# Optimization experiments

Measured on AMD Instinct MI355X. Metric: run time of the kernel, lower is better.

## Reference

```python
import jax, jax.numpy as jnp
import numpy as np

SCALE = 64 ** (-0.5)  # dim_head**-0.5; heads/dim_head otherwise unused in forward


def setup_inputs() -> dict:
    key = jax.random.key(0)
    ks = jax.random.split(key, 7)
    B, C, T = 8, 512, 4096
    s = C ** (-0.5)  # conv1d default init scale-ish
    x = jax.random.normal(ks[0], (B, C, T), dtype=jnp.float32)
    Wq = jax.random.normal(ks[1], (C, C), dtype=jnp.float32) * s
    bq = jax.random.normal(ks[2], (C,), dtype=jnp.float32) * s
    Wk = jax.random.normal(ks[3], (C, C), dtype=jnp.float32) * s
    bk = jax.random.normal(ks[4], (C,), dtype=jnp.float32) * s
    Wv = jax.random.normal(ks[5], (C, C), dtype=jnp.float32) * s
    bv = jax.random.normal(ks[6], (C,), dtype=jnp.float32) * s
    return {"x": x, "Wq": Wq, "bq": bq, "Wk": Wk, "bk": bk, "Wv": Wv, "bv": bv}


def reference(x, Wq, bq, Wk, bk, Wv, bv):
    # 1x1 Conv1d == per-timestep linear over channels: (o,c) x (b,c,t) -> (b,o,t)
    q = jnp.einsum('oc,bct->bot', Wq, x) + bq[None, :, None]
    k = jnp.einsum('oc,bct->bot', Wk, x) + bk[None, :, None]
    v = jnp.einsum('oc,bct->bot', Wv, x) + bv[None, :, None]
    # Channel-channel attention: dots (b, C, C); softmax over last (channel) axis
    dots = jnp.einsum('bct,bdt->bcd', q, k) * SCALE
    attn = jax.nn.softmax(dots, axis=-1)
    # (b,C,C) x (b,C,t) -> (b,C,t); dropout p=0 and to_out unused in original forward
    out = jnp.einsum('bcd,bdt->bct', attn, v)
    return out
```

## Files before the change

kernel.cpp:

```cpp
#include <hip/hip_runtime.h>

#define B_ 8
#define C_ 512
#define T_ 4096

typedef __attribute__((ext_vector_type(8))) __bf16 bf16x8;
typedef __attribute__((ext_vector_type(8))) _Float16 f16x8;
typedef __attribute__((ext_vector_type(8))) unsigned short u16x8;
typedef __attribute__((ext_vector_type(4))) float f32x4;

__device__ __forceinline__ unsigned short f2bf(float f) {
  unsigned int u = __float_as_uint(f);
  u += 0x7fffu + ((u >> 16) & 1u);
  return (unsigned short)(u >> 16);
}
__device__ __forceinline__ float bf2f(unsigned short h) {
  return __uint_as_float(((unsigned int)h) << 16);
}
__device__ __forceinline__ unsigned short f2h(float f) {
  return __builtin_bit_cast(unsigned short, (_Float16)f);
}

__device__ __forceinline__ void async16(unsigned short* ldsdst, const unsigned short* gsrc) {
  __builtin_amdgcn_global_load_lds(
      (__attribute__((address_space(1))) void*)(void*)const_cast<unsigned short*>(gsrc),
      (__attribute__((address_space(3))) void*)(void*)ldsdst,
      16, 0, 0);
}

template <bool F16>
__device__ __forceinline__ f32x4 mfma16(u16x8 a, u16x8 b, f32x4 c) {
  if constexpr (F16)
    return __builtin_amdgcn_mfma_f32_16x16x32_f16(
        __builtin_bit_cast(f16x8, a), __builtin_bit_cast(f16x8, b), c, 0, 0, 0);
  else
    return __builtin_amdgcn_mfma_f32_16x16x32_bf16(
        __builtin_bit_cast(bf16x8, a), __builtin_bit_cast(bf16x8, b), c, 0, 0, 0);
}

struct GemmP {
  const unsigned short* Ah; const unsigned short* Al; long sA; int lda;
  const unsigned short* Bh; const unsigned short* Bl; long sB; int ldb;
  float* Cf; unsigned short* Ch; unsigned short* Cl; long sC; int ldc;
  int kspan; int zparts;
  const float* rowv; const float* colv; const float* bq; const float* bk;
};

enum { EPI_F32 = 0, EPI_OUT = 1, EPI_DOTS = 2, EPI_SPLIT = 3, EPI_F16 = 4 };

template <int BM, int BN, int WM, int WN, bool SA, bool SB, int EPI, bool F16, int SWZ>
__global__ __launch_bounds__((BM / WM) * (BN / WN) * 64) void gemm_nt(GemmP g) {
  constexpr int KC = 64;
  constexpr int NWAVE = (BM / WM) * (BN / WN);
  constexpr int NT = NWAVE * 64;
  constexpr int ASZ = BM * KC, BSZ = BN * KC;
  constexpr int STAGE = (SA ? 2 : 1) * ASZ + (SB ? 2 : 1) * BSZ;
  constexpr int EPAD = BN + 4;
  constexpr int EPIB = 32 * EPAD * 4;
  constexpr int LDSB = (STAGE * 2 > EPIB) ? STAGE * 2 : EPIB;
  __shared__ alignas(16) char ldsraw[LDSB];
  unsigned short* lds = (unsigned short*)ldsraw;
  unsigned short* ldsAh = lds;
  unsigned short* ldsAl = lds + ASZ;
  unsigned short* ldsBh = lds + (SA ? 2 : 1) * ASZ;
  unsigned short* ldsBl = ldsBh + BSZ;

  const int tid = threadIdx.x;
  const int lane = tid & 63, wid = tid >> 6;
  constexpr int WNB = BN / WN;
  const int wm = wid / WNB, wn = wid % WNB;
  constexpr int MF = WM / 16, NF = WN / 16;

  int bm, bn, z;
  if constexpr (SWZ == 1) {
    const int blk = blockIdx.x;
    const int r = blk & 7, q = blk >> 3;
    const int idx = ((r >> 2) * 40) + q;
    const int tri = idx % 10;
    const int tm = (tri >= 6) ? 3 : (tri >= 3) ? 2 : (tri >= 1) ? 1 : 0;
    bm = tm; bn = tri - (tm * (tm + 1)) / 2;
    z = (idx / 10) * 4 + (r & 3);
  } else if constexpr (SWZ == 2) {
    const int blk = blockIdx.x;
    const int r = blk & 7, q = blk >> 3;
    bm = q & 3;
    const int w = q >> 2;
    bn = ((w & 1) << 3) + r;
    z = w >> 1;
  } else {
    bm = blockIdx.x; bn = blockIdx.y; z = blockIdx.z;
  }
  const int b = z / g.zparts, kp = z - b * g.zparts;

  const unsigned short* Ah = g.Ah + (size_t)b * g.sA + (size_t)kp * g.kspan;
  const unsigned short* Al = SA ? (g.Al + (size_t)b * g.sA + (size_t)kp * g.kspan) : nullptr;
  const unsigned short* Bh = g.Bh + (size_t)b * g.sB + (size_t)kp * g.kspan;
  const unsigned short* Bl = SB ? (g.Bl + (size_t)b * g.sB + (size_t)kp * g.kspan) : nullptr;

  f32x4 acc[MF][NF] = {};

  const int kIters = g.kspan / KC;
  for (int kt = 0; kt < kIters; ++kt) {
    const int kb = kt * KC;
#pragma unroll
    for (int r = 0; r < ASZ / (8 * NT); ++r) {
      int idx = tid + r * NT;
      int row = idx >> 3, sl = idx & 7;
      int kc = (sl ^ (row & 7)) << 3;
      size_t goff = (size_t)(bm * BM + row) * g.lda + kb + kc;
      async16(&ldsAh[idx << 3], Ah + goff);
      if constexpr (SA) async16(&ldsAl[idx << 3], Al + goff);
    }
#pragma unroll
    for (int r = 0; r < BSZ / (8 * NT); ++r) {
      int idx = tid + r * NT;
      int row = idx >> 3, sl = idx & 7;
      int kc = (sl ^ (row & 7)) << 3;
      size_t goff = (size_t)(bn * BN + row) * g.ldb + kb + kc;
      async16(&ldsBh[idx << 3], Bh + goff);
      if constexpr (SB) async16(&ldsBl[idx << 3], Bl + goff);
    }
    __syncthreads();

    const int rsel = lane & 15, kq = lane >> 4;
#pragma unroll
    for (int ks = 0; ks < KC; ks += 32) {
      const int chunk = (ks >> 3) + kq;
      u16x8 afh[MF], afl[MF], bfh[NF], bfl[NF];
#pragma unroll
      for (int fm = 0; fm < MF; ++fm) {
        int row = wm * WM + fm * 16 + rsel;
        int ro = row * KC + ((chunk ^ (row & 7)) << 3);
        afh[fm] = *(const u16x8*)&ldsAh[ro];
        if constexpr (SA) afl[fm] = *(const u16x8*)&ldsAl[ro];
      }
#pragma unroll
      for (int fn = 0; fn < NF; ++fn) {
        int row = wn * WN + fn * 16 + rsel;
        int ro = row * KC + ((chunk ^ (row & 7)) << 3);
        bfh[fn] = *(const u16x8*)&ldsBh[ro];
        if constexpr (SB) bfl[fn] = *(const u16x8*)&ldsBl[ro];
      }
#pragma unroll
      for (int fm = 0; fm < MF; ++fm)
#pragma unroll
        for (int fn = 0; fn < NF; ++fn) {
          acc[fm][fn] = mfma16<F16>(afh[fm], bfh[fn], acc[fm][fn]);
          if constexpr (SB) acc[fm][fn] = mfma16<F16>(afh[fm], bfl[fn], acc[fm][fn]);
          if constexpr (SA) acc[fm][fn] = mfma16<F16>(afl[fm], bfh[fn], acc[fm][fn]);
        }
    }
    __syncthreads();
  }

  if constexpr (EPI == EPI_SPLIT || EPI == EPI_F16) {
#pragma unroll
    for (int fm = 0; fm < MF; ++fm)
#pragma unroll
      for (int fn = 0; fn < NF; ++fn)
#pragma unroll
        for (int r = 0; r < 4; ++r) {
          int i = bm * BM + wm * WM + fm * 16 + ((lane >> 4) << 2) + r;
          int j = bn * BN + wn * WN + fn * 16 + (lane & 15);
          float v = acc[fm][fn][r];
          size_t co = (size_t)z * g.sC + (size_t)i * g.ldc + j;
          if constexpr (EPI == EPI_SPLIT) {
            unsigned short h = f2bf(v);
            g.Ch[co] = h;
            g.Cl[co] = f2bf(v - bf2f(h));
          } else {
            g.Ch[co] = f2h(v);
          }
        }
  } else {
    float* eb = (float*)ldsraw;
#pragma unroll
    for (int ck = 0; ck < BM / 32; ++ck) {
      if (wm == (ck * 32) / WM) {
        const int fm0 = ((ck * 32) % WM) / 16;
#pragma unroll
        for (int fi = 0; fi < 2; ++fi) {
          int fm = fm0 + fi;
#pragma unroll
          for (int fn = 0; fn < NF; ++fn)
#pragma unroll
            for (int r = 0; r < 4; ++r) {
              int lrow = fi * 16 + ((lane >> 4) << 2) + r;
              int col = wn * WN + fn * 16 + (lane & 15);
              eb[lrow * EPAD + col] = acc[fm][fn][r];
            }
        }
      }
      __syncthreads();
#pragma unroll
      for (int it = 0; it < (32 * BN / 4) / NT; ++it) {
        int idx = it * NT + tid;
        int row = idx / (BN / 4), c4 = (idx % (BN / 4)) * 4;
        f32x4 v = *(f32x4*)&eb[row * EPAD + c4];
        int grow = bm * BM + ck * 32 + row;
        int j = bn * BN + c4;
        if constexpr (EPI == EPI_OUT) v = v + g.rowv[b * C_ + grow];
        if constexpr (EPI == EPI_DOTS) {
          f32x4 bkv = *(const f32x4*)&g.bk[j];
          f32x4 ksv = *(const f32x4*)&g.colv[b * C_ + j];
          float qsi = g.rowv[b * C_ + grow], bqi = g.bq[grow];
          v = 0.125f * (v + qsi * bkv + bqi * (ksv + 4096.f * bkv));
        }
        __builtin_nontemporal_store(
            v, (f32x4*)&g.Cf[(size_t)z * g.sC + (size_t)grow * g.ldc + j]);
      }
      __syncthreads();
    }
  }
}

#define NXB2 1024
#define PAD 66
__global__ __launch_bounds__(256) void prep_fused(
    const float* __restrict__ x, const float* __restrict__ Wq,
    const float* __restrict__ Wk, const float* __restrict__ Wv,
    unsigned short* __restrict__ Xh, unsigned short* __restrict__ XhT,
    unsigned short* Wqh, unsigned short* Wql,
    unsigned short* Wkh, unsigned short* Wkl, unsigned short* WvT,
    float* __restrict__ S) {
  __shared__ unsigned short tile[64 * PAD];
  const int tid = threadIdx.x;
  if (blockIdx.x < NXB2) {
    const int tl = blockIdx.x;
    const int tb = tl & 15, c0 = ((tl >> 4) & 7) << 6, b = tl >> 7;
    const int t0 = tb << 8;
    const float* xin = x + ((size_t)(b * C_ + c0)) * T_ + t0;
    unsigned short* xo = Xh + ((size_t)(b * C_ + c0)) * T_ + t0;
    const int row16 = tid >> 4, c4 = (tid & 15) << 2;
    float rs[4] = {};
    float4 v[4];
#pragma unroll
    for (int r = 0; r < 4; ++r)
      v[r] = *(const float4*)&xin[(size_t)(row16 + r * 16) * T_ + c4];
    for (int st = 0; st < 4; ++st) {
      if (st) __syncthreads();
#pragma unroll
      for (int r = 0; r < 4; ++r) {
        int row = row16 + r * 16;
        _Float16 q0 = (_Float16)v[r].x, q1 = (_Float16)v[r].y,
                 q2 = (_Float16)v[r].z, q3 = (_Float16)v[r].w;
        unsigned short h0 = __builtin_bit_cast(unsigned short, q0),
                       h1 = __builtin_bit_cast(unsigned short, q1),
                       h2 = __builtin_bit_cast(unsigned short, q2),
                       h3 = __builtin_bit_cast(unsigned short, q3);
        rs[r] += (float)q0 + (float)q1 + (float)q2 + (float)q3;
        ushort4 hv; hv.x = h0; hv.y = h1; hv.z = h2; hv.w = h3;
        *(ushort4*)&xo[(size_t)row * T_ + st * 64 + c4] = hv;
        unsigned int lo = (unsigned int)h0 | ((unsigned int)h1 << 16);
        unsigned int hi = (unsigned int)h2 | ((unsigned int)h3 << 16);
        ((unsigned int*)&tile[row * PAD + c4])[0] = lo;
        ((unsigned int*)&tile[row * PAD + c4])[1] = hi;
      }
      float4 nv[4];
      if (st < 3) {
#pragma unroll
        for (int r = 0; r < 4; ++r)
          nv[r] = *(const float4*)&xin[(size_t)(row16 + r * 16) * T_ + (st + 1) * 64 + c4];
      }
      __syncthreads();
#pragma unroll
      for (int r = 0; r < 2; ++r) {
        int idx = tid + r * 256;
        int trow = idx >> 3, cc = (idx & 7) << 3;
        unsigned short vals[8];
#pragma unroll
        for (int j = 0; j < 8; ++j) vals[j] = tile[(cc + j) * PAD + trow];
        *(uint4*)&XhT[((size_t)b * T_ + t0 + st * 64 + trow) * C_ + c0 + cc] =
            *(uint4*)vals;
      }
#pragma unroll
      for (int r = 0; r < 4; ++r) v[r] = nv[r];
    }
#pragma unroll
    for (int rr = 0; rr < 4; ++rr) {
      float s = rs[rr];
      s += __shfl_down(s, 8, 16);
      s += __shfl_down(s, 4, 16);
      s += __shfl_down(s, 2, 16);
      s += __shfl_down(s, 1, 16);
      if ((tid & 15) == 0) atomicAdd(&S[(b << 9) + c0 + row16 + rr * 16], s);
    }
  } else {
    int i = (blockIdx.x - NXB2) * 256 + tid;
    float q = Wq[i]; unsigned short qh = f2bf(q); Wqh[i] = qh; Wql[i] = f2bf(q - bf2f(qh));
    float k = Wk[i]; unsigned short kh = f2bf(k); Wkh[i] = kh; Wkl[i] = f2bf(k - bf2f(kh));
    float v = Wv[i]; int d = i >> 9, e = i & 511;
    WvT[(e << 9) + d] = f2h(v);
  }
}

__global__ __launch_bounds__(256) void combine_g(const float* __restrict__ gp,
                                                 unsigned short* __restrict__ gh,
                                                 unsigned short* __restrict__ gl) {
  __shared__ float tile[64 * 65];
  const int blk = blockIdx.x;
  const int b = blk & 7, q = blk >> 3;
  const int tr = q >> 3, tc = q & 7;
  const bool mirror = (tr >> 1) < (tc >> 1);
  const int sr = mirror ? tc : tr, sc = mirror ? tr : tc;
  const float* src = gp + ((size_t)b << 20) + (size_t)(sr << 6) * 512 + (sc << 6);
  const int row = threadIdx.x >> 4, c4 = (threadIdx.x & 15) << 2;
  float vals[4][4];
#pragma unroll
  for (int rr = 0; rr < 4; ++rr) {
    const int r = row + rr * 16;
    f32x4 v = {};
#pragma unroll
    for (int p = 0; p < 4; ++p)
      v += __builtin_nontemporal_load(
          (const f32x4*)&src[((size_t)p << 18) + (size_t)r * 512 + c4]);
    if (mirror) {
#pragma unroll
      for (int k = 0; k < 4; ++k) tile[r * 65 + c4 + k] = v[k];
    } else {
#pragma unroll
      for (int k = 0; k < 4; ++k) vals[rr][k] = v[k];
    }
  }
  if (mirror) {
    __syncthreads();
#pragma unroll
    for (int rr = 0; rr < 4; ++rr) {
      const int r = row + rr * 16;
#pragma unroll
      for (int k = 0; k < 4; ++k) vals[rr][k] = tile[(c4 + k) * 65 + r];
    }
  }
  unsigned short* ghp = gh + ((size_t)b << 18) + (size_t)(tr << 6) * 512 + (tc << 6);
  unsigned short* glp = gl + ((size_t)b << 18) + (size_t)(tr << 6) * 512 + (tc << 6);
#pragma unroll
  for (int rr = 0; rr < 4; ++rr) {
    const int r = row + rr * 16;
    ushort4 h, l;
    h.x = f2bf(vals[rr][0]); l.x = f2bf(vals[rr][0] - bf2f(h.x));
    h.y = f2bf(vals[rr][1]); l.y = f2bf(vals[rr][1] - bf2f(h.y));
    h.z = f2bf(vals[rr][2]); l.z = f2bf(vals[rr][2] - bf2f(h.z));
    h.w = f2bf(vals[rr][3]); l.w = f2bf(vals[rr][3] - bf2f(h.w));
    *(ushort4*)&ghp[(size_t)r * 512 + c4] = h;
    *(ushort4*)&glp[(size_t)r * 512 + c4] = l;
  }
}

__global__ __launch_bounds__(256) void qs_ks(const float* __restrict__ Wq, const float* __restrict__ Wk,
                                             const float* __restrict__ s, float* __restrict__ qs,
                                             float* __restrict__ ks) {
  int lane = threadIdx.x & 63, wid = threadIdx.x >> 6;
  int gi = blockIdx.x * 4 + wid;
  int b = gi >> 9, i = gi & 511;
  const float* sv = s + (b << 9);
  const float* wqr = Wq + (size_t)i * C_;
  const float* wkr = Wk + (size_t)i * C_;
  float aq = 0.f, ak = 0.f;
#pragma unroll
  for (int c = lane; c < C_; c += 64) {
    float sc = sv[c];
    aq += wqr[c] * sc;
    ak += wkr[c] * sc;
  }
#pragma unroll
  for (int o = 32; o > 0; o >>= 1) { aq += __shfl_down(aq, o); ak += __shfl_down(ak, o); }
  if (lane == 0) { qs[gi] = aq; ks[gi] = ak; }
}

__global__ __launch_bounds__(256) void softmax_rows(const float* __restrict__ logits,
                                                    const float* __restrict__ bv,
                                                    unsigned short* __restrict__ attn,
                                                    float* __restrict__ ab) {
  const int row = blockIdx.x;
  const int tid = threadIdx.x, lane = tid & 63, wid = tid >> 6;
  const float* L = logits + (size_t)row * C_;
  float v0 = __builtin_nontemporal_load(&L[tid]);
  float v1 = __builtin_nontemporal_load(&L[tid + 256]);
  __shared__ float red[4];
  float m = fmaxf(v0, v1);
#pragma unroll
  for (int o = 32; o > 0; o >>= 1) m = fmaxf(m, __shfl_down(m, o));
  if (lane == 0) red[wid] = m;
  __syncthreads();
  m = fmaxf(fmaxf(red[0], red[1]), fmaxf(red[2], red[3]));
  __syncthreads();
  float e0 = __expf(v0 - m), e1 = __expf(v1 - m);
  float sum = e0 + e1;
#pragma unroll
  for (int o = 32; o > 0; o >>= 1) sum += __shfl_down(sum, o);
  if (lane == 0) red[wid] = sum;
  __syncthreads();
  sum = red[0] + red[1] + red[2] + red[3];
  float inv = 1.f / sum;
  float a0 = e0 * inv, a1 = e1 * inv;
  unsigned short* ar = attn + (size_t)row * C_;
  ar[tid] = f2h(a0);
  ar[tid + 256] = f2h(a1);
  float abv = a0 * bv[tid] + a1 * bv[tid + 256];
  __syncthreads();
#pragma unroll
  for (int o = 32; o > 0; o >>= 1) abv += __shfl_down(abv, o);
  if (lane == 0) red[wid] = abv;
  __syncthreads();
  if (tid == 0) ab[row] = red[0] + red[1] + red[2] + red[3];
}

extern "C" void kernel_launch(void* const* d_in, const int* in_sizes, int n_in,
                              void* d_out, int out_size, void* d_ws, size_t ws_size,
                              hipStream_t stream) {
  const float* x  = (const float*)d_in[0];
  const float* Wq = (const float*)d_in[1];
  const float* bq = (const float*)d_in[2];
  const float* Wk = (const float*)d_in[3];
  const float* bk = (const float*)d_in[4];
  const float* Wv = (const float*)d_in[5];
  const float* bv = (const float*)d_in[6];
  float* out = (float*)d_out;

  char* ws = (char*)d_ws;
  size_t off = 0;
  auto alloc = [&](size_t bytes) {
    char* p = ws + off;
    off += (bytes + 255) & ~(size_t)255;
    return p;
  };
  const size_t XSZ = (size_t)B_ * C_ * T_;
  const size_t GSZ = (size_t)B_ * C_ * C_;

  unsigned short* Xh  = (unsigned short*)alloc(XSZ * 2);
  unsigned short* XhT = (unsigned short*)alloc(XSZ * 2);
  float* Gpart = (float*)alloc((size_t)4 * GSZ * 4);
  unsigned short* Gh = (unsigned short*)alloc(GSZ * 2);
  unsigned short* Gl = (unsigned short*)alloc(GSZ * 2);
  unsigned short* Ph = (unsigned short*)alloc(GSZ * 2);
  unsigned short* Pl = (unsigned short*)alloc(GSZ * 2);
  float* Logits = (float*)alloc(GSZ * 4);
  unsigned short* Attn = (unsigned short*)alloc(GSZ * 2);
  unsigned short* Mh = (unsigned short*)alloc(GSZ * 2);
  unsigned short* Wqh = (unsigned short*)alloc((size_t)C_ * C_ * 2);
  unsigned short* Wql = (unsigned short*)alloc((size_t)C_ * C_ * 2);
  unsigned short* Wkh = (unsigned short*)alloc((size_t)C_ * C_ * 2);
  unsigned short* Wkl = (unsigned short*)alloc((size_t)C_ * C_ * 2);
  unsigned short* WvT = (unsigned short*)alloc((size_t)C_ * C_ * 2);
  float* S  = (float*)alloc((size_t)B_ * C_ * 4);
  float* Qs = (float*)alloc((size_t)B_ * C_ * 4);
  float* Ks = (float*)alloc((size_t)B_ * C_ * 4);
  float* Ab = (float*)alloc((size_t)B_ * C_ * 4);

  hipMemsetAsync(S, 0, (size_t)B_ * C_ * 4, stream);
  prep_fused<<<NXB2 + C_ * C_ / 256, 256, 0, stream>>>(x, Wq, Wk, Wv, Xh, XhT,
                                                       Wqh, Wql, Wkh, Wkl, WvT, S);
  qs_ks<<<B_ * C_ / 4, 256, 0, stream>>>(Wq, Wk, S, Qs, Ks);

  {
    GemmP p = {};
    p.Ah = Xh; p.sA = (long)C_ * T_; p.lda = T_;
    p.Bh = Xh; p.sB = (long)C_ * T_; p.ldb = T_;
    p.Cf = Gpart; p.sC = (long)C_ * C_; p.ldc = C_;
    p.kspan = T_ / 4; p.zparts = 4;
    gemm_nt<128, 128, 32, 64, false, false, EPI_F32, true, 1>
        <<<320, 512, 0, stream>>>(p);
  }
  combine_g<<<B_ * 64, 256, 0, stream>>>(Gpart, Gh, Gl);

  {
    GemmP p = {};
    p.Ah = Wqh; p.Al = Wql; p.sA = 0; p.lda = C_;
    p.Bh = Gh; p.Bl = Gl; p.sB = (long)C_ * C_; p.ldb = C_;
    p.Ch = Ph; p.Cl = Pl; p.sC = (long)C_ * C_; p.ldc = C_;
    p.kspan = C_; p.zparts = 1;
    gemm_nt<64, 64, 32, 32, true, true, EPI_SPLIT, false, 0>
        <<<dim3(8, 8, 8), 256, 0, stream>>>(p);
  }
  {
    GemmP p = {};
    p.Ah = Ph; p.Al = Pl; p.sA = (long)C_ * C_; p.lda = C_;
    p.Bh = Wkh; p.Bl = Wkl; p.sB = 0; p.ldb = C_;
    p.Cf = Logits; p.sC = (long)C_ * C_; p.ldc = C_;
    p.kspan = C_; p.zparts = 1;
    p.rowv = Qs; p.colv = Ks; p.bq = bq; p.bk = bk;
    gemm_nt<64, 64, 32, 32, true, true, EPI_DOTS, false, 0>
        <<<dim3(8, 8, 8), 256, 0, stream>>>(p);
  }
  softmax_rows<<<B_ * C_, 256, 0, stream>>>(Logits, bv, Attn, Ab);
  {
    GemmP p = {};
    p.Ah = Attn; p.sA = (long)C_ * C_; p.lda = C_;
    p.Bh = WvT; p.sB = 0; p.ldb = C_;
    p.Ch = Mh; p.sC = (long)C_ * C_; p.ldc = C_;
    p.kspan = C_; p.zparts = 1;
    gemm_nt<64, 64, 32, 32, false, false, EPI_F16, true, 0>
        <<<dim3(8, 8, 8), 256, 0, stream>>>(p);
  }
  {
    GemmP p = {};
    p.Ah = Mh; p.sA = (long)C_ * C_; p.lda = C_;
    p.Bh = XhT; p.sB = (long)C_ * T_; p.ldb = C_;
    p.Cf = out; p.sC = (long)C_ * T_; p.ldc = T_;
    p.kspan = C_; p.zparts = 1;
    p.rowv = Ab;
    gemm_nt<128, 256, 64, 64, false, false, EPI_OUT, true, 2>
        <<<512, 512, 0, stream>>>(p);
  }
  (void)in_sizes; (void)n_in; (void)out_size; (void)ws_size;
}
```

Baseline: 233.7 us.

## Double-buffer LDS stages in gemm_nt and retile output GEMM to 128x128

Adds a two-stage LDS ping-pong so the next K-chunk's async global-to-LDS loads are issued before the current chunk's MFMA work, letting memory latency overlap compute. The LDS footprint doubles for every gemm_nt instantiation, which may lower occupancy. The final output GEMM also moves from 128x256 tiles on 512 blocks to 128x128 tiles on 1024 blocks, with a matching block-index swizzle. The barrier structure needs care: the loop body shown no longer has a barrier right after the prefetch, so correctness depends on the trailing __syncthreads and on waiting for the async copies.

```diff
diff --git a/kernel.cpp b/kernel.cpp
--- a/kernel.cpp
+++ b/kernel.cpp
@@ -57,13 +57,9 @@
   constexpr int STAGE = (SA ? 2 : 1) * ASZ + (SB ? 2 : 1) * BSZ;
   constexpr int EPAD = BN + 4;
   constexpr int EPIB = 32 * EPAD * 4;
-  constexpr int LDSB = (STAGE * 2 > EPIB) ? STAGE * 2 : EPIB;
+  constexpr int LDSB = (STAGE * 4 > EPIB) ? STAGE * 4 : EPIB;
   __shared__ alignas(16) char ldsraw[LDSB];
   unsigned short* lds = (unsigned short*)ldsraw;
-  unsigned short* ldsAh = lds;
-  unsigned short* ldsAl = lds + ASZ;
-  unsigned short* ldsBh = lds + (SA ? 2 : 1) * ASZ;
-  unsigned short* ldsBl = ldsBh + BSZ;
 
   const int tid = threadIdx.x;
   const int lane = tid & 63, wid = tid >> 6;
@@ -83,10 +79,9 @@
   } else if constexpr (SWZ == 2) {
     const int blk = blockIdx.x;
     const int r = blk & 7, q = blk >> 3;
-    bm = q & 3;
-    const int w = q >> 2;
-    bn = ((w & 1) << 3) + r;
-    z = w >> 1;
+    bn = ((q & 3) << 3) + r;
+    bm = (q >> 2) & 3;
+    z = q >> 4;
   } else {
     bm = blockIdx.x; bn = blockIdx.y; z = blockIdx.z;
   }
@@ -97,19 +92,19 @@
   const unsigned short* Bh = g.Bh + (size_t)b * g.sB + (size_t)kp * g.kspan;
   const unsigned short* Bl = SB ? (g.Bl + (size_t)b * g.sB + (size_t)kp * g.kspan) : nullptr;
 
-  f32x4 acc[MF][NF] = {};
-
-  const int kIters = g.kspan / KC;
-  for (int kt = 0; kt < kIters; ++kt) {
-    const int kb = kt * KC;
+  auto stage = [&](int half, int kb) {
+    unsigned short* dAh = lds + half * STAGE;
+    unsigned short* dAl = dAh + ASZ;
+    unsigned short* dBh = dAh + (SA ? 2 : 1) * ASZ;
+    unsigned short* dBl = dBh + BSZ;
 #pragma unroll
     for (int r = 0; r < ASZ / (8 * NT); ++r) {
       int idx = tid + r * NT;
       int row = idx >> 3, sl = idx & 7;
       int kc = (sl ^ (row & 7)) << 3;
       size_t goff = (size_t)(bm * BM + row) * g.lda + kb + kc;
-      async16(&ldsAh[idx << 3], Ah + goff);
-      if constexpr (SA) async16(&ldsAl[idx << 3], Al + goff);
+      async16(&dAh[idx << 3], Ah + goff);
+      if constexpr (SA) async16(&dAl[idx << 3], Al + goff);
     }
 #pragma unroll
     for (int r = 0; r < BSZ / (8 * NT); ++r) {
@@ -117,10 +112,23 @@
       int row = idx >> 3, sl = idx & 7;
       int kc = (sl ^ (row & 7)) << 3;
       size_t goff = (size_t)(bn * BN + row) * g.ldb + kb + kc;
-      async16(&ldsBh[idx << 3], Bh + goff);
-      if constexpr (SB) async16(&ldsBl[idx << 3], Bl + goff);
-    }
-    __syncthreads();
+      async16(&dBh[idx << 3], Bh + goff);
+      if constexpr (SB) async16(&dBl[idx << 3], Bl + goff);
+    }
+  };
+
+  f32x4 acc[MF][NF] = {};
+
+  const int kIters = g.kspan / KC;
+  stage(0, 0);
+  __syncthreads();
+  for (int kt = 0; kt < kIters; ++kt) {
+    if (kt + 1 < kIters) stage((kt + 1) & 1, (kt + 1) * KC);
+
+    const unsigned short* cAh = lds + (kt & 1) * STAGE;
+    const unsigned short* cAl = cAh + ASZ;
+    const unsigned short* cBh = cAh + (SA ? 2 : 1) * ASZ;
+    const unsigned short* cBl = cBh + BSZ;
 
     const int rsel = lane & 15, kq = lane >> 4;
 #pragma unroll
@@ -131,15 +139,15 @@
       for (int fm = 0; fm < MF; ++fm) {
         int row = wm * WM + fm * 16 + rsel;
         int ro = row * KC + ((chunk ^ (row & 7)) << 3);
-        afh[fm] = *(const u16x8*)&ldsAh[ro];
-        if constexpr (SA) afl[fm] = *(const u16x8*)&ldsAl[ro];
+        afh[fm] = *(const u16x8*)&cAh[ro];
+        if constexpr (SA) afl[fm] = *(const u16x8*)&cAl[ro];
       }
 #pragma unroll
       for (int fn = 0; fn < NF; ++fn) {
         int row = wn * WN + fn * 16 + rsel;
         int ro = row * KC + ((chunk ^ (row & 7)) << 3);
-        bfh[fn] = *(const u16x8*)&ldsBh[ro];
-        if constexpr (SB) bfl[fn] = *(const u16x8*)&ldsBl[ro];
+        bfh[fn] = *(const u16x8*)&cBh[ro];
+        if constexpr (SB) bfl[fn] = *(const u16x8*)&cBl[ro];
       }
 #pragma unroll
       for (int fm = 0; fm < MF; ++fm)
@@ -499,8 +507,8 @@
     p.Cf = out; p.sC = (long)C_ * T_; p.ldc = T_;
     p.kspan = C_; p.zparts = 1;
     p.rowv = Ab;
-    gemm_nt<128, 256, 64, 64, false, false, EPI_OUT, true, 2>
-        <<<512, 512, 0, stream>>>(p);
+    gemm_nt<128, 128, 32, 64, false, false, EPI_OUT, true, 2>
+        <<<1024, 512, 0, stream>>>(p);
   }
   (void)in_sizes; (void)n_in; (void)out_size; (void)ws_size;
 }
```

New measurement: 229.6 us. Within noise of the previous version (-1.7%).
